# Kernel tuning notes

Measured on AMD Instinct MI355X. Metric: run time of the kernel, lower is better.

Reference implementation:

```python
import jax, jax.numpy as jnp
import numpy as np

B, S, D, H = 2, 2048, 1024, 16
DEPTH = D // H


def setup_inputs() -> dict:
    key = jax.random.key(0)
    ks = jax.random.split(key, 12)
    def dense_init(kw, kb, fan_in, fan_out):
        lim = float(np.sqrt(6.0 / (fan_in + fan_out)))
        W = jax.random.uniform(kw, (fan_in, fan_out), jnp.float32, -lim, lim)
        b = jnp.zeros((fan_out,), jnp.float32)
        return W, b
    Wq, bq = dense_init(ks[0], ks[1], D, D)
    Wk, bk = dense_init(ks[2], ks[3], D, D)
    Wv, bv = dense_init(ks[4], ks[5], D, D)
    Wo, bo = dense_init(ks[6], ks[7], D, D)
    return {
        "v": jax.random.normal(ks[8], (B, S, D), jnp.float32),
        "k": jax.random.normal(ks[9], (B, S, D), jnp.float32),
        "q": jax.random.normal(ks[10], (B, S, D), jnp.float32),
        "mask": jnp.zeros((B, 1, 1, S), jnp.float32),
        "Wq": Wq, "bq": bq, "Wk": Wk, "bk": bk,
        "Wv": Wv, "bv": bv, "Wo": Wo, "bo": bo,
    }


def _split_heads(x):
    # (B, S, D) -> (B, H, S, depth)
    b, s, _ = x.shape
    return x.reshape(b, s, H, DEPTH).transpose(0, 2, 1, 3)


def reference(v, k, q, mask, Wq, bq, Wk, bk, Wv, bv, Wo, bo):
    qh = _split_heads(q @ Wq + bq)  # (B,H,S,depth)
    kh = _split_heads(k @ Wk + bk)
    vh = _split_heads(v @ Wv + bv)

    scale = 1.0 / jnp.sqrt(jnp.float32(DEPTH))
    logits = jnp.einsum('bhqd,bhkd->bhqk', qh, kh) * scale  # (B,H,S,S)

    s = logits.shape[-1]
    look_ahead = jnp.triu(jnp.ones((s, s), jnp.float32), k=1)  # 1 above diag
    m = jnp.maximum(mask, look_ahead)  # broadcast (B,1,1,S) vs (S,S)
    logits = logits + m * (-1e17)

    attn = jax.nn.softmax(logits, axis=-1)
    out = jnp.einsum('bhqk,bhkd->bhqd', attn, vh)  # (B,H,S,depth)
    out = out.transpose(0, 2, 1, 3).reshape(q.shape[0], -1, D)  # (B,S,D)
    out = out @ Wo + bo
    return out, attn
```

## Files before the change

kernel.cpp:

```cpp
#include <hip/hip_runtime.h>
#include <hip/hip_bf16.h>

#define BB 2
#define SS 2048
#define DD 1024
#define HH 16
#define DEP 64

typedef short bf16x8 __attribute__((ext_vector_type(8)));
typedef float f32x4 __attribute__((ext_vector_type(4)));
typedef unsigned short us8 __attribute__((ext_vector_type(8)));

static __device__ __forceinline__ unsigned short f2bf(float f) {
    unsigned int u = __float_as_uint(f);
    u += 0x7FFFu + ((u >> 16) & 1u);
    return (unsigned short)(u >> 16);
}

__device__ __forceinline__ void gl_lds16(const void* g, void* l) {
    __builtin_amdgcn_global_load_lds(
        (const __attribute__((address_space(1))) unsigned int*)g,
        (__attribute__((address_space(3))) unsigned int*)l, 16, 0, 0);
}

__device__ __forceinline__ void lds_fence() {
    asm volatile("s_waitcnt lgkmcnt(0)" ::: "memory");
}

__global__ __launch_bounds__(256) void conv_bf16(
    const float* __restrict__ q, const float* __restrict__ k,
    const float* __restrict__ v, unsigned short* __restrict__ qb,
    unsigned short* __restrict__ kb, unsigned short* __restrict__ vb)
{
    const int z = blockIdx.z;
    const float* src = (z == 0) ? q : (z == 1) ? k : v;
    unsigned short* dst = (z == 0) ? qb : (z == 1) ? kb : vb;
    size_t i = ((size_t)blockIdx.x * 256 + threadIdx.x) * 8;
    float4 a = *(const float4*)(src + i);
    float4 b = *(const float4*)(src + i + 4);
    us8 o;
    o[0] = f2bf(a.x); o[1] = f2bf(a.y); o[2] = f2bf(a.z); o[3] = f2bf(a.w);
    o[4] = f2bf(b.x); o[5] = f2bf(b.y); o[6] = f2bf(b.z); o[7] = f2bf(b.w);
    *(us8*)(dst + i) = o;
}

__global__ __launch_bounds__(256) void trans_w(
    const float* __restrict__ Wq, const float* __restrict__ Wk,
    const float* __restrict__ Wv, const float* __restrict__ Wo,
    unsigned short* __restrict__ Wt)
{
    __shared__ unsigned short T[64][72];
    const int z = blockIdx.z;
    const float* W = (z == 0) ? Wq : (z == 1) ? Wk : (z == 2) ? Wv : Wo;
    unsigned short* D = Wt + (size_t)z * 1024 * 1024;
    const int k0 = blockIdx.y * 64, n0 = blockIdx.x * 64;
    const int t = threadIdx.x;
    #pragma unroll
    for (int it = 0; it < 4; ++it) {
        int id = t + it * 256;
        int kk = id >> 4;
        int nn = (id & 15) * 4;
        float4 x = *(const float4*)(W + (size_t)(k0 + kk) * 1024 + n0 + nn);
        T[kk][nn + 0] = f2bf(x.x); T[kk][nn + 1] = f2bf(x.y);
        T[kk][nn + 2] = f2bf(x.z); T[kk][nn + 3] = f2bf(x.w);
    }
    __syncthreads();
    #pragma unroll
    for (int it = 0; it < 2; ++it) {
        int id = t + it * 256;
        int nn = id >> 3;
        int c8 = (id & 7) * 8;
        us8 o;
        #pragma unroll
        for (int j = 0; j < 8; ++j) o[j] = T[c8 + j][nn];
        *(us8*)(D + (size_t)(n0 + nn) * 1024 + k0 + c8) = o;
    }
}

template <int MODE>
__device__ __forceinline__ void gemm_bt_body(
    const unsigned short* __restrict__ A, const unsigned short* __restrict__ Bt,
    const float* __restrict__ bias, unsigned short* __restrict__ OutB,
    float* __restrict__ OutF)
{
    __shared__ unsigned short As[128 * 32];
    __shared__ unsigned short Bs[128 * 32];
    const int t = threadIdx.x;
    const int m0 = blockIdx.y * 128, n0 = blockIdx.x * 128;
    const int w = t >> 6, lane = t & 63, g = lane >> 4, li = lane & 15;
    const int wr = (w & 1) * 64, wc = (w >> 1) * 64;
    const int lrow = lane >> 2, lcol = (lane & 3) * 8;

    f32x4 acc[4][4] = {};

    for (int k0 = 0; k0 < 1024; k0 += 32) {
        #pragma unroll
        for (int i = 0; i < 2; ++i) {
            int c = w * 2 + i;
            int row = c * 16 + lrow;
            gl_lds16(A  + (size_t)(m0 + row) * 1024 + k0 + lcol, As + c * 512);
            gl_lds16(Bt + (size_t)(n0 + row) * 1024 + k0 + lcol, Bs + c * 512);
        }
        __syncthreads();
        bf16x8 af[4], bfr[4];
        #pragma unroll
        for (int i = 0; i < 4; ++i)
            af[i] = *(const bf16x8*)&As[(wr + i * 16 + li) * 32 + g * 8];
        #pragma unroll
        for (int j = 0; j < 4; ++j)
            bfr[j] = *(const bf16x8*)&Bs[(wc + j * 16 + li) * 32 + g * 8];
        #pragma unroll
        for (int i = 0; i < 4; ++i)
            #pragma unroll
            for (int j = 0; j < 4; ++j)
                acc[i][j] = __builtin_amdgcn_mfma_f32_16x16x32_bf16(
                    af[i], bfr[j], acc[i][j], 0, 0, 0);
        __syncthreads();
    }

    #pragma unroll
    for (int i = 0; i < 4; ++i) {
        #pragma unroll
        for (int j = 0; j < 4; ++j) {
            int n = n0 + wc + j * 16 + li;
            float bv = bias[n];
            #pragma unroll
            for (int r = 0; r < 4; ++r) {
                int m = m0 + wr + i * 16 + g * 4 + r;
                float val = acc[i][j][r] + bv;
                if (MODE == 0) {
                    int b = m >> 11, s = m & 2047, h = n >> 6, dd = n & 63;
                    OutB[(((size_t)(b * HH + h)) * SS + s) * DEP + dd] = f2bf(val);
                } else {
                    OutF[(size_t)m * 1024 + n] = val;
                }
            }
        }
    }
}

__global__ __launch_bounds__(256) void gemm_qkv(
    const unsigned short* __restrict__ qb, const unsigned short* __restrict__ kb,
    const unsigned short* __restrict__ vb, const unsigned short* __restrict__ Wt,
    const float* __restrict__ bq, const float* __restrict__ bk,
    const float* __restrict__ bv,
    unsigned short* __restrict__ Qh, unsigned short* __restrict__ Kh,
    unsigned short* __restrict__ Vh)
{
    const int z = blockIdx.z;
    const unsigned short* A = (z == 0) ? qb : (z == 1) ? kb : vb;
    const unsigned short* B = Wt + (size_t)z * 1024 * 1024;
    const float* bi = (z == 0) ? bq : (z == 1) ? bk : bv;
    unsigned short* O = (z == 0) ? Qh : (z == 1) ? Kh : Vh;
    gemm_bt_body<0>(A, B, bi, O, nullptr);
}

__global__ __launch_bounds__(256) void gemm_o(
    const unsigned short* __restrict__ A, const unsigned short* __restrict__ Wt,
    const float* __restrict__ bo, float* __restrict__ Out)
{
    gemm_bt_body<1>(A, Wt + (size_t)3 * 1024 * 1024, bo, nullptr, Out);
}

__global__ __launch_bounds__(256) void transpose_v(
    const unsigned short* __restrict__ Vh, unsigned short* __restrict__ Vt)
{
    __shared__ unsigned short T[64][65];
    const int bh = blockIdx.y;
    const int s0 = blockIdx.x * 64;
    const int t = threadIdx.x;
    #pragma unroll
    for (int c = 0; c < 2; ++c) {
        int id = t + c * 256;
        int row = id >> 3, col8 = (id & 7) * 8;
        us8 v = *(const us8*)(Vh + ((size_t)bh * SS + s0 + row) * DEP + col8);
        #pragma unroll
        for (int i = 0; i < 8; ++i) T[row][col8 + i] = v[i];
    }
    __syncthreads();
    #pragma unroll
    for (int c = 0; c < 2; ++c) {
        int id = t + c * 256;
        int d = id >> 3, col8 = (id & 7) * 8;
        us8 v;
        #pragma unroll
        for (int i = 0; i < 8; ++i) v[i] = T[col8 + i][d];
        *(us8*)(Vt + ((size_t)bh * DEP + d) * SS + s0 + col8) = v;
    }
}

__global__ __launch_bounds__(256) void attn_kernel(
    const unsigned short* __restrict__ Qh, const unsigned short* __restrict__ Kh,
    const unsigned short* __restrict__ Vt, const float* __restrict__ mask,
    float* __restrict__ attn, unsigned short* __restrict__ out_h)
{
    __shared__ float Pf[4][16 * 36];
    const int bh = blockIdx.y;
    const int b = bh >> 4, h = bh & 15;
    const int t = threadIdx.x;
    const int w = t >> 6, lane = t & 63, g = lane >> 4, li = lane & 15;
    const int x = blockIdx.x;
    const int r0 = (w < 2) ? (x * 32 + w * 16) : (SS - 32 - x * 32 + (w - 2) * 16);
    const float scale = 0.125f;

    const unsigned short* Qb = Qh + (size_t)bh * SS * DEP;
    const unsigned short* Kb = Kh + (size_t)bh * SS * DEP;
    const unsigned short* Vb = Vt + (size_t)bh * DEP * SS;
    float* attn_b = attn + (size_t)bh * SS * SS;
    const float* mask_b = mask + (size_t)b * SS;

    bf16x8 aQ0 = *(const bf16x8*)(Qb + (size_t)(r0 + li) * DEP + g * 8);
    bf16x8 aQ1 = *(const bf16x8*)(Qb + (size_t)(r0 + li) * DEP + 32 + g * 8);

    float m_[4], l_[4];
    #pragma unroll
    for (int r = 0; r < 4; ++r) { m_[r] = -1e30f; l_[r] = 0.0f; }

    const int nch = ((r0 + 15) >> 6) + 1;
    for (int ch = 0; ch < nch; ++ch) {
        int cb = ch * 64;
        f32x4 c[4];
        #pragma unroll
        for (int tt = 0; tt < 4; ++tt) {
            const unsigned short* Kp = Kb + (size_t)(cb + tt * 16 + li) * DEP + g * 8;
            bf16x8 k0v = *(const bf16x8*)Kp;
            bf16x8 k1v = *(const bf16x8*)(Kp + 32);
            f32x4 z = {};
            z = __builtin_amdgcn_mfma_f32_16x16x32_bf16(aQ0, k0v, z, 0, 0, 0);
            z = __builtin_amdgcn_mfma_f32_16x16x32_bf16(aQ1, k1v, z, 0, 0, 0);
            c[tt] = z;
        }
        float mv[4];
        #pragma unroll
        for (int tt = 0; tt < 4; ++tt) mv[tt] = mask_b[cb + tt * 16 + li];
        #pragma unroll
        for (int r = 0; r < 4; ++r) {
            int row = r0 + g * 4 + r;
            float s[4];
            #pragma unroll
            for (int tt = 0; tt < 4; ++tt) {
                int col = cb + tt * 16 + li;
                float pen = fmaxf(mv[tt], (col > row) ? 1.0f : 0.0f);
                s[tt] = c[tt][r] * scale + pen * (-1e17f);
            }
            float cm = fmaxf(fmaxf(s[0], s[1]), fmaxf(s[2], s[3]));
            cm = fmaxf(cm, __shfl_xor(cm, 1));
            cm = fmaxf(cm, __shfl_xor(cm, 2));
            cm = fmaxf(cm, __shfl_xor(cm, 4));
            cm = fmaxf(cm, __shfl_xor(cm, 8));
            float mn = fmaxf(m_[r], cm);
            float ps = __expf(s[0] - mn) + __expf(s[1] - mn) +
                       __expf(s[2] - mn) + __expf(s[3] - mn);
            ps += __shfl_xor(ps, 1);
            ps += __shfl_xor(ps, 2);
            ps += __shfl_xor(ps, 4);
            ps += __shfl_xor(ps, 8);
            l_[r] = l_[r] * __expf(m_[r] - mn) + ps;
            m_[r] = mn;
        }
    }
    float rl[4];
    #pragma unroll
    for (int r = 0; r < 4; ++r) rl[r] = 1.0f / l_[r];

    f32x4 o[4] = {};
    float* Pw = Pf[w];
    const int jjc = ((r0 + 15) >> 5) + 1;
    for (int jj = 0; jj < jjc; ++jj) {
        int cb = jj * 32;
        bf16x8 vf[4];
        #pragma unroll
        for (int tt = 0; tt < 4; ++tt)
            vf[tt] = *(const bf16x8*)(Vb + (size_t)(tt * 16 + li) * SS + cb + g * 8);
        #pragma unroll
        for (int hh = 0; hh < 2; ++hh) {
            int ct = cb + hh * 16;
            const unsigned short* Kp = Kb + (size_t)(ct + li) * DEP + g * 8;
            bf16x8 k0v = *(const bf16x8*)Kp;
            bf16x8 k1v = *(const bf16x8*)(Kp + 32);
            f32x4 c = {};
            c = __builtin_amdgcn_mfma_f32_16x16x32_bf16(aQ0, k0v, c, 0, 0, 0);
            c = __builtin_amdgcn_mfma_f32_16x16x32_bf16(aQ1, k1v, c, 0, 0, 0);
            float mv = mask_b[ct + li];
            #pragma unroll
            for (int r = 0; r < 4; ++r) {
                int row = r0 + g * 4 + r;
                float pen = fmaxf(mv, (ct + li > row) ? 1.0f : 0.0f);
                float s = c[r] * scale + pen * (-1e17f);
                Pw[(g * 4 + r) * 36 + hh * 16 + li] = __expf(s - m_[r]) * rl[r];
            }
        }
        lds_fence();
        #pragma unroll
        for (int it = 0; it < 2; ++it) {
            int rloc = it * 8 + (lane >> 3);
            int c4 = (lane & 7) * 4;
            f32x4 val = *(const f32x4*)&Pw[rloc * 36 + c4];
            __builtin_nontemporal_store(
                val, (f32x4*)(attn_b + (size_t)(r0 + rloc) * SS + cb + c4));
        }
        float pf[8];
        *(f32x4*)&pf[0] = *(const f32x4*)&Pw[li * 36 + g * 8];
        *(f32x4*)&pf[4] = *(const f32x4*)&Pw[li * 36 + g * 8 + 4];
        bf16x8 aP;
        #pragma unroll
        for (int i = 0; i < 8; ++i) aP[i] = (short)f2bf(pf[i]);
        #pragma unroll
        for (int tt = 0; tt < 4; ++tt)
            o[tt] = __builtin_amdgcn_mfma_f32_16x16x32_bf16(aP, vf[tt], o[tt], 0, 0, 0);
        lds_fence();
    }

    for (int cb = jjc * 32; cb < SS; cb += 64) {
        int col = cb + li * 4;
        if (col < SS) {
            f32x4 z4 = {0.f, 0.f, 0.f, 0.f};
            #pragma unroll
            for (int r = 0; r < 4; ++r) {
                int row = r0 + g * 4 + r;
                __builtin_nontemporal_store(
                    z4, (f32x4*)(attn_b + (size_t)row * SS + col));
            }
        }
    }

    unsigned short* Ow = (unsigned short*)Pw;
    #pragma unroll
    for (int tt = 0; tt < 4; ++tt)
        #pragma unroll
        for (int r = 0; r < 4; ++r)
            Ow[(g * 4 + r) * 72 + tt * 16 + li] = f2bf(o[tt][r]);
    lds_fence();
    #pragma unroll
    for (int it = 0; it < 2; ++it) {
        int rloc = it * 8 + (lane >> 3);
        int c8 = (lane & 7) * 8;
        us8 val = *(const us8*)&Ow[rloc * 72 + c8];
        *(us8*)(out_h + ((size_t)b * SS + r0 + rloc) * DD + h * DEP + c8) = val;
    }
}

extern "C" void kernel_launch(void* const* d_in, const int* in_sizes, int n_in,
                              void* d_out, int out_size, void* d_ws, size_t ws_size,
                              hipStream_t stream) {
    const float* v    = (const float*)d_in[0];
    const float* k    = (const float*)d_in[1];
    const float* q    = (const float*)d_in[2];
    const float* mask = (const float*)d_in[3];
    const float* Wq   = (const float*)d_in[4];
    const float* bq   = (const float*)d_in[5];
    const float* Wk   = (const float*)d_in[6];
    const float* bk   = (const float*)d_in[7];
    const float* Wv   = (const float*)d_in[8];
    const float* bv   = (const float*)d_in[9];
    const float* Wo   = (const float*)d_in[10];
    const float* bo   = (const float*)d_in[11];

    char* ws = (char*)d_ws;
    const size_t MB = 1 << 20;
    unsigned short* qb   = (unsigned short*)(ws + 0 * MB);
    unsigned short* kb   = (unsigned short*)(ws + 8 * MB);
    unsigned short* vb   = (unsigned short*)(ws + 16 * MB);
    unsigned short* Qh   = (unsigned short*)(ws + 24 * MB);
    unsigned short* Kh   = (unsigned short*)(ws + 32 * MB);
    unsigned short* Vh   = (unsigned short*)(ws + 40 * MB);
    unsigned short* Wt   = (unsigned short*)(ws + 48 * MB);
    unsigned short* out_h = qb;
    unsigned short* Vt    = kb;

    float* out_f = (float*)d_out;
    float* attn  = out_f + (size_t)BB * SS * DD;

    conv_bf16<<<dim3(2048, 1, 3), 256, 0, stream>>>(q, k, v, qb, kb, vb);
    trans_w<<<dim3(16, 16, 4), 256, 0, stream>>>(Wq, Wk, Wv, Wo, Wt);
    gemm_qkv<<<dim3(8, 32, 3), 256, 0, stream>>>(qb, kb, vb, Wt, bq, bk, bv,
                                                 Qh, Kh, Vh);
    transpose_v<<<dim3(32, 32), 256, 0, stream>>>(Vh, Vt);
    attn_kernel<<<dim3(32, 32), 256, 0, stream>>>(Qh, Kh, Vt, mask, attn, out_h);
    gemm_o<<<dim3(8, 32), 256, 0, stream>>>(out_h, Wt, bo, out_f);
}
```

Measured before the change: 814.6 us.

## Double-buffer GEMM LDS tiles and prefetch K fragments in attention loop

The projection GEMM now uses two LDS buffers, issuing the global-to-LDS loads for the next k-tile before computing the current one, with explicit vmcnt waits and raw barriers replacing __syncthreads. The attention kernel prefetches the next iteration's K fragments into registers and double-buffers the per-wave P scratch in LDS, which removes the trailing LDS fence. The aim is to hide global load latency behind MFMA work. In exchange it uses twice the LDS and more registers, which may lower occupancy, and the hand-written waitcnt count has to match the number of outstanding loads exactly.

```diff
diff --git a/kernel.cpp b/kernel.cpp
--- a/kernel.cpp
+++ b/kernel.cpp
@@ -83,40 +83,52 @@
     const float* __restrict__ bias, unsigned short* __restrict__ OutB,
     float* __restrict__ OutF)
 {
-    __shared__ unsigned short As[128 * 32];
-    __shared__ unsigned short Bs[128 * 32];
+    __shared__ unsigned short As[2][128 * 32];
+    __shared__ unsigned short Bs[2][128 * 32];
     const int t = threadIdx.x;
     const int m0 = blockIdx.y * 128, n0 = blockIdx.x * 128;
     const int w = t >> 6, lane = t & 63, g = lane >> 4, li = lane & 15;
     const int wr = (w & 1) * 64, wc = (w >> 1) * 64;
     const int lrow = lane >> 2, lcol = (lane & 3) * 8;
+    const int c0 = w * 2, c1 = w * 2 + 1;
+    const int row0 = c0 * 16 + lrow, row1 = c1 * 16 + lrow;
 
     f32x4 acc[4][4] = {};
 
-    for (int k0 = 0; k0 < 1024; k0 += 32) {
-        #pragma unroll
-        for (int i = 0; i < 2; ++i) {
-            int c = w * 2 + i;
-            int row = c * 16 + lrow;
-            gl_lds16(A  + (size_t)(m0 + row) * 1024 + k0 + lcol, As + c * 512);
-            gl_lds16(Bt + (size_t)(n0 + row) * 1024 + k0 + lcol, Bs + c * 512);
-        }
-        __syncthreads();
+    auto stage = [&](int buf, int k0) {
+        gl_lds16(A  + (size_t)(m0 + row0) * 1024 + k0 + lcol, &As[buf][c0 * 512]);
+        gl_lds16(A  + (size_t)(m0 + row1) * 1024 + k0 + lcol, &As[buf][c1 * 512]);
+        gl_lds16(Bt + (size_t)(n0 + row0) * 1024 + k0 + lcol, &Bs[buf][c0 * 512]);
+        gl_lds16(Bt + (size_t)(n0 + row1) * 1024 + k0 + lcol, &Bs[buf][c1 * 512]);
+    };
+    auto compute = [&](int buf) {
         bf16x8 af[4], bfr[4];
         #pragma unroll
         for (int i = 0; i < 4; ++i)
-            af[i] = *(const bf16x8*)&As[(wr + i * 16 + li) * 32 + g * 8];
+            af[i] = *(const bf16x8*)&As[buf][(wr + i * 16 + li) * 32 + g * 8];
         #pragma unroll
         for (int j = 0; j < 4; ++j)
-            bfr[j] = *(const bf16x8*)&Bs[(wc + j * 16 + li) * 32 + g * 8];
+            bfr[j] = *(const bf16x8*)&Bs[buf][(wc + j * 16 + li) * 32 + g * 8];
         #pragma unroll
         for (int i = 0; i < 4; ++i)
             #pragma unroll
             for (int j = 0; j < 4; ++j)
                 acc[i][j] = __builtin_amdgcn_mfma_f32_16x16x32_bf16(
                     af[i], bfr[j], acc[i][j], 0, 0, 0);
-        __syncthreads();
-    }
+    };
+
+    stage(0, 0);
+    for (int k0 = 0; k0 < 1024 - 32; k0 += 32) {
+        const int cur = (k0 >> 5) & 1;
+        stage(cur ^ 1, k0 + 32);
+        asm volatile("s_waitcnt vmcnt(4)" ::: "memory");
+        __builtin_amdgcn_s_barrier();
+        compute(cur);
+        __builtin_amdgcn_s_barrier();
+    }
+    asm volatile("s_waitcnt vmcnt(0)" ::: "memory");
+    __builtin_amdgcn_s_barrier();
+    compute(1);
 
     #pragma unroll
     for (int i = 0; i < 4; ++i) {
@@ -194,7 +206,7 @@
     const unsigned short* __restrict__ Vt, const float* __restrict__ mask,
     float* __restrict__ attn, unsigned short* __restrict__ out_h)
 {
-    __shared__ float Pf[4][16 * 36];
+    __shared__ float Pf[4][2][16 * 36];
     const int bh = blockIdx.y;
     const int b = bh >> 4, h = bh & 15;
     const int t = threadIdx.x;
@@ -264,23 +276,35 @@
     for (int r = 0; r < 4; ++r) rl[r] = 1.0f / l_[r];
 
     f32x4 o[4] = {};
-    float* Pw = Pf[w];
     const int jjc = ((r0 + 15) >> 5) + 1;
+
+    bf16x8 kc[4], kn[4];
+    {
+        const unsigned short* Kp0 = Kb + (size_t)(0 + li) * DEP + g * 8;
+        const unsigned short* Kp1 = Kb + (size_t)(16 + li) * DEP + g * 8;
+        kc[0] = *(const bf16x8*)Kp0; kc[1] = *(const bf16x8*)(Kp0 + 32);
+        kc[2] = *(const bf16x8*)Kp1; kc[3] = *(const bf16x8*)(Kp1 + 32);
+    }
+
     for (int jj = 0; jj < jjc; ++jj) {
         int cb = jj * 32;
+        float* Pw = &Pf[w][jj & 1][0];
         bf16x8 vf[4];
         #pragma unroll
         for (int tt = 0; tt < 4; ++tt)
             vf[tt] = *(const bf16x8*)(Vb + (size_t)(tt * 16 + li) * SS + cb + g * 8);
+        if (jj + 1 < jjc) {
+            const unsigned short* Kp0 = Kb + (size_t)(cb + 32 + li) * DEP + g * 8;
+            const unsigned short* Kp1 = Kb + (size_t)(cb + 48 + li) * DEP + g * 8;
+            kn[0] = *(const bf16x8*)Kp0; kn[1] = *(const bf16x8*)(Kp0 + 32);
+            kn[2] = *(const bf16x8*)Kp1; kn[3] = *(const bf16x8*)(Kp1 + 32);
+        }
         #pragma unroll
         for (int hh = 0; hh < 2; ++hh) {
             int ct = cb + hh * 16;
-            const unsigned short* Kp = Kb + (size_t)(ct + li) * DEP + g * 8;
-            bf16x8 k0v = *(const bf16x8*)Kp;
-            bf16x8 k1v = *(const bf16x8*)(Kp + 32);
             f32x4 c = {};
-            c = __builtin_amdgcn_mfma_f32_16x16x32_bf16(aQ0, k0v, c, 0, 0, 0);
-            c = __builtin_amdgcn_mfma_f32_16x16x32_bf16(aQ1, k1v, c, 0, 0, 0);
+            c = __builtin_amdgcn_mfma_f32_16x16x32_bf16(aQ0, kc[hh * 2 + 0], c, 0, 0, 0);
+            c = __builtin_amdgcn_mfma_f32_16x16x32_bf16(aQ1, kc[hh * 2 + 1], c, 0, 0, 0);
             float mv = mask_b[ct + li];
             #pragma unroll
             for (int r = 0; r < 4; ++r) {
@@ -308,7 +332,7 @@
         #pragma unroll
         for (int tt = 0; tt < 4; ++tt)
             o[tt] = __builtin_amdgcn_mfma_f32_16x16x32_bf16(aP, vf[tt], o[tt], 0, 0, 0);
-        lds_fence();
+        kc[0] = kn[0]; kc[1] = kn[1]; kc[2] = kn[2]; kc[3] = kn[3];
     }
 
     for (int cb = jjc * 32; cb < SS; cb += 64) {
@@ -324,7 +348,7 @@
         }
     }
 
-    unsigned short* Ow = (unsigned short*)Pw;
+    unsigned short* Ow = (unsigned short*)&Pf[w][0][0];
     #pragma unroll
     for (int tt = 0; tt < 4; ++tt)
         #pragma unroll
```

After: 789.1 us. 1.03x faster.
